# Kernel optimization log

Hardware: AMD Instinct MI355X
Metric: run time of the kernel (lower is better)

Reference implementation:

```python
import jax, jax.numpy as jnp
import numpy as np

SRC_LEN, TGT_LEN, BATCH = 256, 128, 256
NH, NE, NSYM = 512, 256, 64


def setup_inputs() -> dict:
    key = jax.random.key(0)
    ks = jax.random.split(key, 14)
    w = lambda k, shape: jax.random.normal(k, shape, jnp.float32) * 0.05
    return {
        "src_enc": jax.random.normal(ks[0], (SRC_LEN, BATCH, NH), jnp.float32),
        "tgt": jax.random.randint(ks[1], (TGT_LEN, BATCH, 1), 0, NSYM, jnp.int32),
        "src_lengths": jax.random.randint(ks[2], (BATCH,), 1, SRC_LEN + 1, jnp.int32),
        "emb_table": w(ks[3], (NSYM, NE)),
        "Ws_w": w(ks[4], (NH, NH)), "Ws_b": jnp.zeros((NH,), jnp.float32),
        "Wz_w": w(ks[5], (NH, NE + 2 * NH)), "Wz_b": jnp.zeros((NH,), jnp.float32),
        "Wr_w": w(ks[6], (NH, NE + 2 * NH)), "Wr_b": jnp.zeros((NH,), jnp.float32),
        "Wn_w": w(ks[7], (NH, NE + 2 * NH)), "Wn_b": jnp.zeros((NH,), jnp.float32),
        "Wa_w": w(ks[8], (NH, 2 * NH)), "Wa_b": jnp.zeros((NH,), jnp.float32),
        "va_w": w(ks[9], (1, NH)),
        "Wo_w": w(ks[10], (NH, NE + 2 * NH)), "Wo_b": jnp.zeros((NH,), jnp.float32),
    }


def reference(src_enc, tgt, src_lengths, emb_table,
              Ws_w, Ws_b, Wz_w, Wz_b, Wr_w, Wr_b, Wn_w, Wn_b,
              Wa_w, Wa_b, va_w, Wo_w, Wo_b):
    src_len, batch, nh = src_enc.shape
    # src_mask: [src_len, batch] True where position < length
    mask = jnp.arange(src_len)[:, None] < src_lengths[None, :]
    tgt_embed = emb_table[tgt[..., 0]]                     # [T, B, E]
    s0 = jnp.tanh(src_enc[0] @ Ws_w.T + Ws_b)              # [B, H]
    # Split Wa into the s-part and src_enc-part; encoder projection is
    # loop-invariant, compute it once (same math as cat+Linear).
    Wa_s, Wa_e = Wa_w[:, :nh], Wa_w[:, nh:]
    enc_proj = jnp.einsum('sbh,gh->sbg', src_enc, Wa_e) + Wa_b  # [S, B, H]
    va = va_w[0]                                           # [H]
    neg_inf = jnp.float32(-jnp.inf)

    def step(s, emb_i):
        h = jnp.tanh(enc_proj + s @ Wa_s.T)                # [S, B, H]
        ei = jnp.einsum('sbh,h->sb', h, va)                # [S, B]
        ei = jnp.where(mask, ei, neg_inf)
        ai = jax.nn.softmax(ei, axis=0)                    # [S, B]
        ci = jnp.einsum('sb,sbh->bh', ai, src_enc)         # [B, H]
        x = jnp.concatenate([emb_i, s, ci], axis=-1)       # [B, E+2H]
        ti = x @ Wo_w.T + Wo_b
        zi = jax.nn.sigmoid(x @ Wz_w.T + Wz_b)
        ri = jax.nn.sigmoid(x @ Wr_w.T + Wr_b)
        xn = jnp.concatenate([emb_i, ri * s, ci], axis=-1)
        ni = jnp.tanh(xn @ Wn_w.T + Wn_b)
        s_new = (1.0 - zi) * s + zi * ni
        return s_new, (ti, s, ai.T)

    _, (dec_outputs, dec_states, dec_attns) = jax.lax.scan(step, s0, tgt_embed[:-1])
    # dec_outputs/dec_states: [T-1, B, H]; dec_attns: [T-1, B, S]
    return dec_outputs, dec_states, dec_attns
```

## Files before the change

### kernel.cpp

```cpp
#include <hip/hip_runtime.h>
#include <hip/hip_bf16.h>
#include <cstdint>
#include <cstddef>

namespace {

constexpr int S_LEN  = 256;
constexpr int BATCH  = 256;
constexpr int NH     = 512;
constexpr int NE     = 256;
constexpr int NSTEPS = 127;
constexpr int N1     = 2048;
constexpr size_t SB        = (size_t)S_LEN * BATCH;
constexpr size_t SRC_ELEMS = SB * NH;

typedef __attribute__((ext_vector_type(8))) short  short8v;
typedef __attribute__((ext_vector_type(4))) float  float4v;
typedef unsigned short us;

constexpr int EPI_EPROJ = 1, EPI_S0 = 4;

__device__ __forceinline__ float bf2f(us u) {
  union { unsigned int i; float f; } c; c.i = ((unsigned int)u) << 16; return c.f;
}
__device__ __forceinline__ us f2bf(float f) {
  union { float f; unsigned int i; } c; c.f = f;
  unsigned int x = c.i;
  return (us)((x + 0x7FFFu + ((x >> 16) & 1u)) >> 16);
}
__device__ __forceinline__ float tanh2(float x) {
  return 1.f - 2.f * __builtin_amdgcn_rcpf(__expf(2.f * x) + 1.f);
}
__device__ __forceinline__ float sigm(float x) {
  return __builtin_amdgcn_rcpf(1.f + __expf(-x));
}
__device__ __forceinline__ void gload16(const us* g, us* l) {
  __builtin_amdgcn_global_load_lds(
      (const __attribute__((address_space(1))) unsigned int*)g,
      (__attribute__((address_space(3))) unsigned int*)l, 16, 0, 0);
}


__global__ void k_conv_src(const float* __restrict__ src, us* __restrict__ dst) {
  const int total = S_LEN * BATCH * 64;
  int i = blockIdx.x * blockDim.x + threadIdx.x;
  int stride = gridDim.x * blockDim.x;
  for (; i < total; i += stride) {
    int c = i & 63, s = (i >> 6) & 255, b = i >> 14;
    const float* p = src + ((size_t)s * BATCH + b) * NH + c * 8;
    float4 v0 = *(const float4*)p;
    float4 v1 = *(const float4*)(p + 4);
    us o[8] = { f2bf(v0.x), f2bf(v0.y), f2bf(v0.z), f2bf(v0.w),
                f2bf(v1.x), f2bf(v1.y), f2bf(v1.z), f2bf(v1.w) };
    *(short8v*)(dst + (size_t)i * 8) = *(const short8v*)o;
  }
}

__global__ void k_conv_w(const float* __restrict__ Wo, const float* __restrict__ Wz,
                         const float* __restrict__ Wr, const float* __restrict__ Wn,
                         const float* __restrict__ Wa, const float* __restrict__ Ws,
                         const float* __restrict__ Wob, const float* __restrict__ Wzb,
                         const float* __restrict__ Wrb, const float* __restrict__ Wnb,
                         us* __restrict__ W1cat, us* __restrict__ Wns,
                         us* __restrict__ Was, us* __restrict__ Wae,
                         us* __restrict__ Wsbf, float* __restrict__ bcat) {
  const int T1 = 2048 * 1280;
  const int T2 = 512 * 512;
  const int total = T1 + 4 * T2 + 2048;
  int i = blockIdx.x * blockDim.x + threadIdx.x;
  int stride = gridDim.x * blockDim.x;
  for (; i < total; i += stride) {
    int idx = i;
    if (idx < T1) {
      int row = idx / 1280, col = idx - row * 1280;
      float v;
      if      (row < 512)  v = Wo[row * 1280 + col];
      else if (row < 1024) v = Wz[(row - 512) * 1280 + col];
      else if (row < 1536) v = Wr[(row - 1024) * 1280 + col];
      else {
        int g = row - 1536;
        v = (col >= 256 && col < 768) ? 0.f : Wn[g * 1280 + col];
      }
      W1cat[idx] = f2bf(v);
    } else if ((idx -= T1) < T2) {
      int g = idx >> 9, j = idx & 511;
      Wns[idx] = f2bf(Wn[g * 1280 + 256 + j]);
    } else if ((idx -= T2) < T2) {
      int g = idx >> 9, h = idx & 511;
      Was[idx] = f2bf(Wa[g * 1024 + h]);
    } else if ((idx -= T2) < T2) {
      int g = idx >> 9, h = idx & 511;
      Wae[idx] = f2bf(Wa[g * 1024 + 512 + h]);
    } else if ((idx -= T2) < T2) {
      Wsbf[idx] = f2bf(Ws[idx]);
    } else {
      idx -= T2;
      bcat[idx] = (idx < 512) ? Wob[idx]
                : (idx < 1024) ? Wzb[idx - 512]
                : (idx < 1536) ? Wrb[idx - 1024]
                               : Wnb[idx - 1536];
    }
  }
}

__global__ void k_emb(const int* __restrict__ tgt, const float* __restrict__ table,
                      us* __restrict__ emb) {
  const int total = NSTEPS * BATCH * NE;
  int i = blockIdx.x * blockDim.x + threadIdx.x;
  int stride = gridDim.x * blockDim.x;
  for (; i < total; i += stride) {
    int e  = i & (NE - 1);
    int tb = i >> 8;
    int sym = tgt[tb];
    emb[i] = f2bf(table[sym * NE + e]);
  }
}

template<int EPI>
__global__ __launch_bounds__(512, 2) void k_gemm(
    const us* __restrict__ A0, int lda, const us* __restrict__ Bw, int ldb, int K,
    const float* __restrict__ bias, float* __restrict__ f0, us* __restrict__ g0) {
  __shared__ alignas(16) char smem[49152];
  char* As0 = smem;
  char* Bs0 = smem + 16384;
  const int tid = threadIdx.x;
  const int m0 = blockIdx.x * 64, n0 = blockIdx.y * 128;
  const int arow = tid >> 3, ac = (tid & 7) * 8;
  const int brow = tid >> 2, bc = (tid & 3) * 16;
  short8v ar, br0, br1;

  auto loadT = [&](int k0) {
    ar = *(const short8v*)(A0 + (size_t)(m0 + arow) * lda + (k0 + ac));
    const us* q = Bw + (size_t)(n0 + brow) * ldb + (k0 + bc);
    br0 = *(const short8v*)q;
    br1 = *(const short8v*)(q + 8);
  };
  auto stage = [&](int buf) {
    *(short8v*)(As0 + buf * 8192 + arow * 128 + ((ac * 2) ^ ((arow & 7) << 4))) = ar;
    char* bb = Bs0 + buf * 16384 + brow * 128;
    const int sw = (brow & 7) << 4;
    *(short8v*)(bb + ((bc * 2) ^ sw)) = br0;
    *(short8v*)(bb + ((bc * 2 + 16) ^ sw)) = br1;
  };

  const int lane = tid & 63, wave = tid >> 6;
  const int wm = (wave >> 2) * 32, wn = (wave & 3) * 32;
  const int fr = lane & 15, kq = lane >> 4;
  const int ra0 = wm + fr, ra1 = ra0 + 16;
  const int rb0 = wn + fr, rb1 = rb0 + 16;
  float4v acc00 = {0,0,0,0}, acc01 = {0,0,0,0}, acc10 = {0,0,0,0}, acc11 = {0,0,0,0};

  loadT(0);
  stage(0);
  const int nit = K >> 6;
  for (int it = 0; it < nit; ++it) {
    __syncthreads();
    if (it + 1 < nit) loadT((it + 1) << 6);
    const char* ab = As0 + (it & 1) * 8192;
    const char* bb = Bs0 + (it & 1) * 16384;
    #pragma unroll
    for (int ks = 0; ks < 2; ++ks) {
      const int cb = ks * 64 + kq * 16;
      short8v a0 = *(const short8v*)(ab + ra0 * 128 + (cb ^ ((ra0 & 7) << 4)));
      short8v a1 = *(const short8v*)(ab + ra1 * 128 + (cb ^ ((ra1 & 7) << 4)));
      short8v b0 = *(const short8v*)(bb + rb0 * 128 + (cb ^ ((rb0 & 7) << 4)));
      short8v b1 = *(const short8v*)(bb + rb1 * 128 + (cb ^ ((rb1 & 7) << 4)));
      acc00 = __builtin_amdgcn_mfma_f32_16x16x32_bf16(a0, b0, acc00, 0, 0, 0);
      acc01 = __builtin_amdgcn_mfma_f32_16x16x32_bf16(a0, b1, acc01, 0, 0, 0);
      acc10 = __builtin_amdgcn_mfma_f32_16x16x32_bf16(a1, b0, acc10, 0, 0, 0);
      acc11 = __builtin_amdgcn_mfma_f32_16x16x32_bf16(a1, b1, acc11, 0, 0, 0);
    }
    if (it + 1 < nit) stage((it + 1) & 1);
  }

  #pragma unroll
  for (int am = 0; am < 2; ++am) {
    #pragma unroll
    for (int bn = 0; bn < 2; ++bn) {
      float4v a = am ? (bn ? acc11 : acc10) : (bn ? acc01 : acc00);
      #pragma unroll
      for (int r = 0; r < 4; ++r) {
        const int rowO = m0 + wm + am * 16 + kq * 4 + r;
        const int colO = n0 + wn + bn * 16 + fr;
        float v = a[r];
        if (EPI == EPI_S0) {
          float tv = tanh2(v + bias[colO]);
          f0[(size_t)rowO * 512 + colO] = tv;
          g0[(size_t)rowO * 512 + colO] = f2bf(tv);
        } else {
          g0[(size_t)rowO * 512 + colO] = f2bf(v + bias[colO]);
        }
      }
    }
  }
}

__global__ __launch_bounds__(512, 1) void k_fused(
    const us* __restrict__ ep,
    const us* __restrict__ src,
    const us* __restrict__ Wns, const us* __restrict__ Was,
    const float* __restrict__ vaw, const int* __restrict__ slen,
    const float* __restrict__ zi, const float* __restrict__ npart,
    const us* __restrict__ xn,
    float* __restrict__ s_f32, us* __restrict__ s_bf, us* __restrict__ ci_bf,
    float* __restrict__ dec_st_t, float* __restrict__ dec_at_t, int has_gru) {
  __shared__ alignas(16) us stg[3][32][512];
  __shared__ float sfl[512];
  __shared__ float q2l[512];
  __shared__ float pl[256];
  __shared__ float lred[8];
  __shared__ float wpart[8][512];
  const int b = blockIdx.x, tid = threadIdx.x;
  const int lane = tid & 63, wv = tid >> 6;
  const int g0l = lane * 8;
  const int len = slen[b];
  const us* epb  = ep  + (size_t)b * S_LEN * NH;
  const us* srcb = src + (size_t)b * S_LEN * NH;

  float vv2[8]; float sumv = 0.f;
  {
    const float* vp = vaw + g0l;
    #pragma unroll
    for (int j = 0; j < 8; j++) { vv2[j] = 2.f * vp[j]; sumv += vp[j]; }
    #pragma unroll
    for (int off = 32; off > 0; off >>= 1) sumv += __shfl_xor(sumv, off, 64);
  }

  auto issue3 = [&](const us* base) {
    #pragma unroll
    for (int c = 0; c < 3; ++c)
      #pragma unroll
      for (int i = 0; i < 4; ++i) {
        int r = wv * 4 + i;
        gload16(base + (size_t)(c * 32 + r) * NH + g0l, &stg[c][r][0]);
      }
  };

  float s_new;
  if (has_gru) {
    float* xnf = &wpart[0][0];
    xnf[tid] = bf2f(xn[b * 512 + tid]);
    __syncthreads();
    issue3(epb);
    const us* wr = Wns + (size_t)tid * 512;
    float acc = 0.f;
    #pragma unroll 8
    for (int k = 0; k < 64; ++k) {
      short8v w8 = ((const short8v*)wr)[k];
      #pragma unroll
      for (int j = 0; j < 8; j++)
        acc = __builtin_fmaf(bf2f((us)w8[j]), xnf[k * 8 + j], acc);
    }
    float z  = zi[b * 512 + tid];
    float so = s_f32[b * 512 + tid];
    float nv = tanh2(npart[b * 512 + tid] + acc);
    s_new = (1.f - z) * so + z * nv;
    s_f32[b * 512 + tid] = s_new;
    s_bf[b * 512 + tid]  = f2bf(s_new);
  } else {
    issue3(epb);
    s_new = s_f32[b * 512 + tid];
  }
  sfl[tid] = s_new;
  __builtin_nontemporal_store(s_new, &dec_st_t[b * 512 + tid]);
  __syncthreads();

  {
    const us* wr = Was + (size_t)tid * 512;
    float acc = 0.f;
    #pragma unroll 8
    for (int k = 0; k < 64; ++k) {
      short8v w8 = ((const short8v*)wr)[k];
      #pragma unroll
      for (int j = 0; j < 8; j++)
        acc = __builtin_fmaf(bf2f((us)w8[j]), sfl[k * 8 + j], acc);
    }
    q2l[tid] = 2.f * acc;
  }
  __syncthreads();

  float q2[8];
  #pragma unroll
  for (int j = 0; j < 8; j++) q2[j] = q2l[g0l + j];
  float lsum = 0.f;
  #pragma unroll
  for (int c = 0; c < 8; ++c) {
    if (c < 6)      asm volatile("s_waitcnt vmcnt(8)" ::: "memory");
    else if (c == 6) asm volatile("s_waitcnt vmcnt(4)" ::: "memory");
    else             asm volatile("s_waitcnt vmcnt(0)" ::: "memory");
    #pragma unroll
    for (int i = 0; i < 4; ++i) {
      const int r = wv * 4 + i;
      const int s = c * 32 + r;
      short8v v = *(const short8v*)&stg[c % 3][r][g0l];
      float acc = 0.f;
      #pragma unroll
      for (int j = 0; j < 8; j++) {
        float arg = __builtin_fmaf(bf2f((us)v[j]), 2.f, q2[j]);
        acc = __builtin_fmaf(vv2[j], __builtin_amdgcn_rcpf(__expf(arg) + 1.f), acc);
      }
      #pragma unroll
      for (int off = 32; off > 0; off >>= 1) acc += __shfl_xor(acc, off, 64);
      float p = (s < len) ? __expf(sumv - acc) : 0.f;
      if (lane == 0) pl[s] = p;
      lsum += p;
    }
    asm volatile("s_waitcnt lgkmcnt(0)" ::: "memory");
    __builtin_amdgcn_sched_barrier(0);
    if (c + 3 < 8) {
      #pragma unroll
      for (int i = 0; i < 4; ++i) {
        const int r = wv * 4 + i;
        gload16(epb + (size_t)((c + 3) * 32 + r) * NH + g0l, &stg[(c + 3) % 3][r][0]);
      }
    }
  }
  if (lane == 0) lred[wv] = lsum;
  __syncthreads();
  float l = 0.f;
  #pragma unroll
  for (int w = 0; w < 8; w++) l += lred[w];
  const float inv = __builtin_amdgcn_rcpf(l);

  if (tid < 256)
    __builtin_nontemporal_store(pl[tid] * inv, &dec_at_t[b * 256 + tid]);
  issue3(srcb);

  float a8[8] = {0,0,0,0,0,0,0,0};
  #pragma unroll
  for (int c = 0; c < 8; ++c) {
    if (c < 6)      asm volatile("s_waitcnt vmcnt(8)" ::: "memory");
    else if (c == 6) asm volatile("s_waitcnt vmcnt(4)" ::: "memory");
    else             asm volatile("s_waitcnt vmcnt(0)" ::: "memory");
    #pragma unroll
    for (int i = 0; i < 4; ++i) {
      const int r = wv * 4 + i;
      const int s = c * 32 + r;
      short8v v = *(const short8v*)&stg[c % 3][r][g0l];
      float pv = pl[s];
      #pragma unroll
      for (int j = 0; j < 8; j++)
        a8[j] = __builtin_fmaf(pv, bf2f((us)v[j]), a8[j]);
    }
    asm volatile("s_waitcnt lgkmcnt(0)" ::: "memory");
    __builtin_amdgcn_sched_barrier(0);
    if (c + 3 < 8) {
      #pragma unroll
      for (int i = 0; i < 4; ++i) {
        const int r = wv * 4 + i;
        gload16(srcb + (size_t)((c + 3) * 32 + r) * NH + g0l, &stg[(c + 3) % 3][r][0]);
      }
    }
  }
  #pragma unroll
  for (int j = 0; j < 8; j++) wpart[wv][g0l + j] = a8[j];
  __syncthreads();
  float cv = 0.f;
  #pragma unroll
  for (int w = 0; w < 8; w++) cv += wpart[w][tid];
  ci_bf[b * 512 + tid] = f2bf(cv * inv);
}

__global__ __launch_bounds__(256, 4) void k_step1(
    const us* __restrict__ emb_t, const us* __restrict__ sbf,
    const us* __restrict__ cibf, const us* __restrict__ W1cat,
    const float* __restrict__ bcat, const float* __restrict__ s_f32,
    float* __restrict__ dec_out_t, float* __restrict__ zi,
    float* __restrict__ npart, us* __restrict__ xn) {
  __shared__ alignas(16) char smem[24576];
  const int bid = blockIdx.x, tid = threadIdx.x;
  const int lane = tid & 63, wv = tid >> 6;
  char* As = smem;
  char* Bs = smem + 8192;
  const int m0 = (bid >> 4) * 64, n0 = (bid & 15) * 128;
  const int fr = lane & 15, kq = lane >> 4;
  const int wm = (wv & 1) * 32, wn0 = (wv >> 1) * 32;
  const int ra0 = wm + fr, ra1 = ra0 + 16;
  float4v acc[2][2][2];
  #pragma unroll
  for (int x = 0; x < 2; x++)
    #pragma unroll
    for (int y = 0; y < 2; y++)
      #pragma unroll
      for (int z = 0; z < 2; z++) acc[x][y][z] = (float4v){0,0,0,0};

  for (int kt = 0; kt < 20; ++kt) {
    __syncthreads();
    #pragma unroll
    for (int j = 0; j < 2; j++) {
      int cid = tid + 256 * j;
      int arow = cid >> 3, ac8 = (cid & 7) * 8;
      int cc = kt * 64 + ac8, rowg = m0 + arow;
      const us* p = (cc < 256) ? emb_t + (size_t)rowg * 256 + cc
                  : (cc < 768) ? sbf + (size_t)rowg * 512 + (cc - 256)
                               : cibf + (size_t)rowg * 512 + (cc - 768);
      *(short8v*)(As + arow * 128 + ((ac8 * 2) ^ ((arow & 7) << 4))) =
          *(const short8v*)p;
    }
    #pragma unroll
    for (int j = 0; j < 4; j++) {
      int cid = tid + 256 * j;
      int brow = cid >> 3, bc8 = (cid & 7) * 8;
      *(short8v*)(Bs + brow * 128 + ((bc8 * 2) ^ ((brow & 7) << 4))) =
          *(const short8v*)(W1cat + (size_t)(n0 + brow) * 1280 + kt * 64 + bc8);
    }
    __syncthreads();
    #pragma unroll
    for (int ks = 0; ks < 2; ++ks) {
      const int cb = ks * 64 + kq * 16;
      short8v a0 = *(const short8v*)(As + ra0 * 128 + (cb ^ ((ra0 & 7) << 4)));
      short8v a1 = *(const short8v*)(As + ra1 * 128 + (cb ^ ((ra1 & 7) << 4)));
      #pragma unroll
      for (int nh = 0; nh < 2; ++nh) {
        const int rb0 = wn0 + nh * 64 + fr, rb1 = rb0 + 16;
        short8v b0 = *(const short8v*)(Bs + rb0 * 128 + (cb ^ ((rb0 & 7) << 4)));
        short8v b1 = *(const short8v*)(Bs + rb1 * 128 + (cb ^ ((rb1 & 7) << 4)));
        acc[nh][0][0] = __builtin_amdgcn_mfma_f32_16x16x32_bf16(a0, b0, acc[nh][0][0], 0, 0, 0);
        acc[nh][0][1] = __builtin_amdgcn_mfma_f32_16x16x32_bf16(a0, b1, acc[nh][0][1], 0, 0, 0);
        acc[nh][1][0] = __builtin_amdgcn_mfma_f32_16x16x32_bf16(a1, b0, acc[nh][1][0], 0, 0, 0);
        acc[nh][1][1] = __builtin_amdgcn_mfma_f32_16x16x32_bf16(a1, b1, acc[nh][1][1], 0, 0, 0);
      }
    }
  }

  #pragma unroll
  for (int nh = 0; nh < 2; ++nh) {
    #pragma unroll
    for (int am = 0; am < 2; ++am) {
      #pragma unroll
      for (int bn = 0; bn < 2; ++bn) {
        #pragma unroll
        for (int r = 0; r < 4; ++r) {
          const int rowO = m0 + wm + am * 16 + kq * 4 + r;
          const int colO = n0 + wn0 + nh * 64 + bn * 16 + fr;
          float v = acc[nh][am][bn][r] + bcat[colO];
          const int qd = colO >> 9, j = colO & 511;
          const size_t idx = (size_t)rowO * 512 + j;
          if      (qd == 0) __builtin_nontemporal_store(v, &dec_out_t[idx]);
          else if (qd == 1) zi[idx] = sigm(v);
          else if (qd == 2) xn[idx] = f2bf(sigm(v) * s_f32[idx]);
          else              npart[idx] = v;
        }
      }
    }
  }
}

}

extern "C" void kernel_launch(void* const* d_in, const int* in_sizes, int n_in,
                              void* d_out, int out_size, void* d_ws, size_t ws_size,
                              hipStream_t stream) {
  const float* src_enc  = (const float*)d_in[0];
  const int*   tgt      = (const int*)d_in[1];
  const int*   slen     = (const int*)d_in[2];
  const float* emb_tab  = (const float*)d_in[3];
  const float* Wsw      = (const float*)d_in[4];
  const float* Wsb      = (const float*)d_in[5];
  const float* Wzw      = (const float*)d_in[6];
  const float* Wzb      = (const float*)d_in[7];
  const float* Wrw      = (const float*)d_in[8];
  const float* Wrb      = (const float*)d_in[9];
  const float* Wnw      = (const float*)d_in[10];
  const float* Wnb      = (const float*)d_in[11];
  const float* Waw      = (const float*)d_in[12];
  const float* Wab      = (const float*)d_in[13];
  const float* vaw      = (const float*)d_in[14];
  const float* Wow      = (const float*)d_in[15];
  const float* Wob      = (const float*)d_in[16];

  char* ws = (char*)d_ws;
  size_t off = 0;
  auto alloc = [&](size_t bytes) -> void* {
    void* p = ws + off;
    off = (off + bytes + 255) & ~(size_t)255;
    return p;
  };
  us*    src_t  = (us*)alloc(SRC_ELEMS * 2);
  us*    ep_t   = (us*)alloc(SRC_ELEMS * 2);
  us*    emb_bf = (us*)alloc((size_t)NSTEPS * BATCH * NE * 2);
  us*    W1cat  = (us*)alloc((size_t)N1 * 1280 * 2);
  us*    Wns    = (us*)alloc((size_t)512 * 512 * 2);
  us*    Was    = (us*)alloc((size_t)512 * 512 * 2);
  us*    Wae    = (us*)alloc((size_t)512 * 512 * 2);
  us*    Wsbf   = (us*)alloc((size_t)512 * 512 * 2);
  float* bcat   = (float*)alloc((size_t)N1 * 4);
  float* s_f32  = (float*)alloc((size_t)BATCH * NH * 4);
  us*    s_bf   = (us*)alloc((size_t)BATCH * NH * 2);
  float* zi     = (float*)alloc((size_t)BATCH * NH * 4);
  float* npart  = (float*)alloc((size_t)BATCH * NH * 4);
  us*    xn_bf  = (us*)alloc((size_t)BATCH * NH * 2);
  us*    ci_bf  = (us*)alloc((size_t)BATCH * NH * 2);

  float* out         = (float*)d_out;
  float* dec_outputs = out;
  float* dec_states  = out + (size_t)NSTEPS * BATCH * NH;
  float* dec_attns   = dec_states + (size_t)NSTEPS * BATCH * NH;

  k_conv_src<<<4096, 256, 0, stream>>>(src_enc, src_t);
  k_conv_w<<<2048, 256, 0, stream>>>(Wow, Wzw, Wrw, Wnw, Waw, Wsw,
                                     Wob, Wzb, Wrb, Wnb,
                                     W1cat, Wns, Was, Wae, Wsbf, bcat);
  k_emb<<<2048, 256, 0, stream>>>(tgt, emb_tab, emb_bf);
  k_gemm<EPI_S0><<<dim3(4, 4), 512, 0, stream>>>(
      src_t, S_LEN * NH, Wsbf, 512, 512, Wsb, s_f32, s_bf);
  k_gemm<EPI_EPROJ><<<dim3(1024, 4), 512, 0, stream>>>(
      src_t, 512, Wae, 512, 512, Wab, nullptr, ep_t);

  for (int t = 0; t < NSTEPS; t++) {
    k_fused<<<BATCH, 512, 0, stream>>>(
        ep_t, src_t, Wns, Was, vaw, slen, zi, npart, xn_bf,
        s_f32, s_bf, ci_bf,
        dec_states + (size_t)t * BATCH * NH,
        dec_attns + (size_t)t * BATCH * S_LEN, t > 0 ? 1 : 0);
    k_step1<<<64, 256, 0, stream>>>(
        emb_bf + (size_t)t * BATCH * NE, s_bf, ci_bf, W1cat, bcat, s_f32,
        dec_outputs + (size_t)t * BATCH * NH, zi, npart, xn_bf);
  }
}
```

Measured before the change: 11.15 ms.

## Interleave encoder projection and source rows; fuse score and context passes

Stores the bf16 encoder projection and the bf16 source encoding side by side in one row of 1024 elements per (batch, position). The attention kernel then reads both in a single pass over positions, computing unnormalised softmax weights and accumulating the context at once, instead of making two passes through LDS-staged async loads. It drops the LDS staging buffers and raises the occupancy hint so more blocks can hide latency with plain register loads. The context is now accumulated with unnormalised exp weights and scaled by the inverse sum afterwards, which is mathematically the same. The cost is losing the explicit async-copy prefetch pipeline.

```diff
diff --git a/kernel.cpp b/kernel.cpp
--- a/kernel.cpp
+++ b/kernel.cpp
@@ -13,6 +13,7 @@
 constexpr int N1     = 2048;
 constexpr size_t SB        = (size_t)S_LEN * BATCH;
 constexpr size_t SRC_ELEMS = SB * NH;
+constexpr int RW = 1024;
 
 typedef __attribute__((ext_vector_type(8))) short  short8v;
 typedef __attribute__((ext_vector_type(4))) float  float4v;
@@ -34,14 +35,9 @@
 __device__ __forceinline__ float sigm(float x) {
   return __builtin_amdgcn_rcpf(1.f + __expf(-x));
 }
-__device__ __forceinline__ void gload16(const us* g, us* l) {
-  __builtin_amdgcn_global_load_lds(
-      (const __attribute__((address_space(1))) unsigned int*)g,
-      (__attribute__((address_space(3))) unsigned int*)l, 16, 0, 0);
-}
-
-
-__global__ void k_conv_src(const float* __restrict__ src, us* __restrict__ dst) {
+
+
+__global__ void k_conv_src(const float* __restrict__ src, us* __restrict__ cat) {
   const int total = S_LEN * BATCH * 64;
   int i = blockIdx.x * blockDim.x + threadIdx.x;
   int stride = gridDim.x * blockDim.x;
@@ -52,7 +48,8 @@
     float4 v1 = *(const float4*)(p + 4);
     us o[8] = { f2bf(v0.x), f2bf(v0.y), f2bf(v0.z), f2bf(v0.w),
                 f2bf(v1.x), f2bf(v1.y), f2bf(v1.z), f2bf(v1.w) };
-    *(short8v*)(dst + (size_t)i * 8) = *(const short8v*)o;
+    *(short8v*)(cat + ((size_t)b * S_LEN + s) * RW + 512 + c * 8) =
+        *(const short8v*)o;
   }
 }
 
@@ -119,7 +116,8 @@
 template<int EPI>
 __global__ __launch_bounds__(512, 2) void k_gemm(
     const us* __restrict__ A0, int lda, const us* __restrict__ Bw, int ldb, int K,
-    const float* __restrict__ bias, float* __restrict__ f0, us* __restrict__ g0) {
+    const float* __restrict__ bias, float* __restrict__ f0, us* __restrict__ g0,
+    int ldc) {
   __shared__ alignas(16) char smem[49152];
   char* As0 = smem;
   char* Bs0 = smem + 16384;
@@ -186,25 +184,23 @@
         if (EPI == EPI_S0) {
           float tv = tanh2(v + bias[colO]);
           f0[(size_t)rowO * 512 + colO] = tv;
-          g0[(size_t)rowO * 512 + colO] = f2bf(tv);
+          g0[(size_t)rowO * ldc + colO] = f2bf(tv);
         } else {
-          g0[(size_t)rowO * 512 + colO] = f2bf(v + bias[colO]);
+          g0[(size_t)rowO * ldc + colO] = f2bf(v + bias[colO]);
         }
       }
     }
   }
 }
 
-__global__ __launch_bounds__(512, 1) void k_fused(
-    const us* __restrict__ ep,
-    const us* __restrict__ src,
+__global__ __launch_bounds__(512, 4) void k_stepA(
+    const us* __restrict__ cat,
     const us* __restrict__ Wns, const us* __restrict__ Was,
     const float* __restrict__ vaw, const int* __restrict__ slen,
     const float* __restrict__ zi, const float* __restrict__ npart,
     const us* __restrict__ xn,
     float* __restrict__ s_f32, us* __restrict__ s_bf, us* __restrict__ ci_bf,
     float* __restrict__ dec_st_t, float* __restrict__ dec_at_t, int has_gru) {
-  __shared__ alignas(16) us stg[3][32][512];
   __shared__ float sfl[512];
   __shared__ float q2l[512];
   __shared__ float pl[256];
@@ -214,8 +210,6 @@
   const int lane = tid & 63, wv = tid >> 6;
   const int g0l = lane * 8;
   const int len = slen[b];
-  const us* epb  = ep  + (size_t)b * S_LEN * NH;
-  const us* srcb = src + (size_t)b * S_LEN * NH;
 
   float vv2[8]; float sumv = 0.f;
   {
@@ -225,23 +219,12 @@
     #pragma unroll
     for (int off = 32; off > 0; off >>= 1) sumv += __shfl_xor(sumv, off, 64);
   }
-
-  auto issue3 = [&](const us* base) {
-    #pragma unroll
-    for (int c = 0; c < 3; ++c)
-      #pragma unroll
-      for (int i = 0; i < 4; ++i) {
-        int r = wv * 4 + i;
-        gload16(base + (size_t)(c * 32 + r) * NH + g0l, &stg[c][r][0]);
-      }
-  };
 
   float s_new;
   if (has_gru) {
     float* xnf = &wpart[0][0];
     xnf[tid] = bf2f(xn[b * 512 + tid]);
     __syncthreads();
-    issue3(epb);
     const us* wr = Wns + (size_t)tid * 512;
     float acc = 0.f;
     #pragma unroll 8
@@ -257,8 +240,8 @@
     s_new = (1.f - z) * so + z * nv;
     s_f32[b * 512 + tid] = s_new;
     s_bf[b * 512 + tid]  = f2bf(s_new);
+    __syncthreads();
   } else {
-    issue3(epb);
     s_new = s_f32[b * 512 + tid];
   }
   sfl[tid] = s_new;
@@ -282,40 +265,55 @@
   float q2[8];
   #pragma unroll
   for (int j = 0; j < 8; j++) q2[j] = q2l[g0l + j];
+
+  const us* cb = cat + (size_t)b * S_LEN * RW + g0l;
   float lsum = 0.f;
-  #pragma unroll
-  for (int c = 0; c < 8; ++c) {
-    if (c < 6)      asm volatile("s_waitcnt vmcnt(8)" ::: "memory");
-    else if (c == 6) asm volatile("s_waitcnt vmcnt(4)" ::: "memory");
-    else             asm volatile("s_waitcnt vmcnt(0)" ::: "memory");
-    #pragma unroll
-    for (int i = 0; i < 4; ++i) {
-      const int r = wv * 4 + i;
-      const int s = c * 32 + r;
-      short8v v = *(const short8v*)&stg[c % 3][r][g0l];
-      float acc = 0.f;
-      #pragma unroll
-      for (int j = 0; j < 8; j++) {
-        float arg = __builtin_fmaf(bf2f((us)v[j]), 2.f, q2[j]);
-        acc = __builtin_fmaf(vv2[j], __builtin_amdgcn_rcpf(__expf(arg) + 1.f), acc);
-      }
-      #pragma unroll
-      for (int off = 32; off > 0; off >>= 1) acc += __shfl_xor(acc, off, 64);
-      float p = (s < len) ? __expf(sumv - acc) : 0.f;
-      if (lane == 0) pl[s] = p;
-      lsum += p;
-    }
-    asm volatile("s_waitcnt lgkmcnt(0)" ::: "memory");
-    __builtin_amdgcn_sched_barrier(0);
-    if (c + 3 < 8) {
-      #pragma unroll
-      for (int i = 0; i < 4; ++i) {
-        const int r = wv * 4 + i;
-        gload16(epb + (size_t)((c + 3) * 32 + r) * NH + g0l, &stg[(c + 3) % 3][r][0]);
-      }
-    }
-  }
+  float c8a = 0.f, c8b = 0.f, c8c = 0.f, c8d = 0.f,
+        c8e = 0.f, c8f = 0.f, c8g = 0.f, c8h = 0.f;
+
+  short8v e0, f0, e1, f1, e2, f2, e3, f3;
+  auto LDR = [&](int i, short8v& ev, short8v& fv) {
+    const us* p = cb + (size_t)(wv + 8 * i) * RW;
+    ev = *(const short8v*)p;
+    fv = *(const short8v*)(p + 512);
+  };
+  auto PROC = [&](int i, short8v& ev, short8v& fv) {
+    const int s = wv + 8 * i;
+    float acc = 0.f;
+    #pragma unroll
+    for (int j = 0; j < 8; j++) {
+      float arg = __builtin_fmaf(bf2f((us)ev[j]), 2.f, q2[j]);
+      acc = __builtin_fmaf(vv2[j], __builtin_amdgcn_rcpf(__expf(arg) + 1.f), acc);
+    }
+    #pragma unroll
+    for (int off = 32; off > 0; off >>= 1) acc += __shfl_xor(acc, off, 64);
+    float p = (s < len) ? __expf(sumv - acc) : 0.f;
+    if (lane == 0) pl[s] = p;
+    lsum += p;
+    c8a = __builtin_fmaf(p, bf2f((us)fv[0]), c8a);
+    c8b = __builtin_fmaf(p, bf2f((us)fv[1]), c8b);
+    c8c = __builtin_fmaf(p, bf2f((us)fv[2]), c8c);
+    c8d = __builtin_fmaf(p, bf2f((us)fv[3]), c8d);
+    c8e = __builtin_fmaf(p, bf2f((us)fv[4]), c8e);
+    c8f = __builtin_fmaf(p, bf2f((us)fv[5]), c8f);
+    c8g = __builtin_fmaf(p, bf2f((us)fv[6]), c8g);
+    c8h = __builtin_fmaf(p, bf2f((us)fv[7]), c8h);
+  };
+
+  LDR(0, e0, f0); LDR(1, e1, f1); LDR(2, e2, f2); LDR(3, e3, f3);
+  for (int i = 0; i < 32; i += 4) {
+    PROC(i + 0, e0, f0); if (i + 4 < 32) LDR(i + 4, e0, f0);
+    PROC(i + 1, e1, f1); if (i + 5 < 32) LDR(i + 5, e1, f1);
+    PROC(i + 2, e2, f2); if (i + 6 < 32) LDR(i + 6, e2, f2);
+    PROC(i + 3, e3, f3); if (i + 7 < 32) LDR(i + 7, e3, f3);
+  }
+
   if (lane == 0) lred[wv] = lsum;
+  {
+    float w0_[8] = { c8a, c8b, c8c, c8d, c8e, c8f, c8g, c8h };
+    #pragma unroll
+    for (int j = 0; j < 8; j++) wpart[wv][g0l + j] = w0_[j];
+  }
   __syncthreads();
   float l = 0.f;
   #pragma unroll
@@ -324,44 +322,14 @@
 
   if (tid < 256)
     __builtin_nontemporal_store(pl[tid] * inv, &dec_at_t[b * 256 + tid]);
-  issue3(srcb);
-
-  float a8[8] = {0,0,0,0,0,0,0,0};
-  #pragma unroll
-  for (int c = 0; c < 8; ++c) {
-    if (c < 6)      asm volatile("s_waitcnt vmcnt(8)" ::: "memory");
-    else if (c == 6) asm volatile("s_waitcnt vmcnt(4)" ::: "memory");
-    else             asm volatile("s_waitcnt vmcnt(0)" ::: "memory");
-    #pragma unroll
-    for (int i = 0; i < 4; ++i) {
-      const int r = wv * 4 + i;
-      const int s = c * 32 + r;
-      short8v v = *(const short8v*)&stg[c % 3][r][g0l];
-      float pv = pl[s];
-      #pragma unroll
-      for (int j = 0; j < 8; j++)
-        a8[j] = __builtin_fmaf(pv, bf2f((us)v[j]), a8[j]);
-    }
-    asm volatile("s_waitcnt lgkmcnt(0)" ::: "memory");
-    __builtin_amdgcn_sched_barrier(0);
-    if (c + 3 < 8) {
-      #pragma unroll
-      for (int i = 0; i < 4; ++i) {
-        const int r = wv * 4 + i;
-        gload16(srcb + (size_t)((c + 3) * 32 + r) * NH + g0l, &stg[(c + 3) % 3][r][0]);
-      }
-    }
-  }
-  #pragma unroll
-  for (int j = 0; j < 8; j++) wpart[wv][g0l + j] = a8[j];
-  __syncthreads();
+
   float cv = 0.f;
   #pragma unroll
   for (int w = 0; w < 8; w++) cv += wpart[w][tid];
   ci_bf[b * 512 + tid] = f2bf(cv * inv);
 }
 
-__global__ __launch_bounds__(256, 4) void k_step1(
+__global__ __launch_bounds__(256, 4) void k_stepB(
     const us* __restrict__ emb_t, const us* __restrict__ sbf,
     const us* __restrict__ cibf, const us* __restrict__ W1cat,
     const float* __restrict__ bcat, const float* __restrict__ s_f32,
@@ -476,8 +444,7 @@
     off = (off + bytes + 255) & ~(size_t)255;
     return p;
   };
-  us*    src_t  = (us*)alloc(SRC_ELEMS * 2);
-  us*    ep_t   = (us*)alloc(SRC_ELEMS * 2);
+  us*    cat    = (us*)alloc(SB * RW * 2);
   us*    emb_bf = (us*)alloc((size_t)NSTEPS * BATCH * NE * 2);
   us*    W1cat  = (us*)alloc((size_t)N1 * 1280 * 2);
   us*    Wns    = (us*)alloc((size_t)512 * 512 * 2);
@@ -497,23 +464,23 @@
   float* dec_states  = out + (size_t)NSTEPS * BATCH * NH;
   float* dec_attns   = dec_states + (size_t)NSTEPS * BATCH * NH;
 
-  k_conv_src<<<4096, 256, 0, stream>>>(src_enc, src_t);
+  k_conv_src<<<4096, 256, 0, stream>>>(src_enc, cat);
   k_conv_w<<<2048, 256, 0, stream>>>(Wow, Wzw, Wrw, Wnw, Waw, Wsw,
                                      Wob, Wzb, Wrb, Wnb,
                                      W1cat, Wns, Was, Wae, Wsbf, bcat);
   k_emb<<<2048, 256, 0, stream>>>(tgt, emb_tab, emb_bf);
   k_gemm<EPI_S0><<<dim3(4, 4), 512, 0, stream>>>(
-      src_t, S_LEN * NH, Wsbf, 512, 512, Wsb, s_f32, s_bf);
+      cat + 512, S_LEN * RW, Wsbf, 512, 512, Wsb, s_f32, s_bf, 512);
   k_gemm<EPI_EPROJ><<<dim3(1024, 4), 512, 0, stream>>>(
-      src_t, 512, Wae, 512, 512, Wab, nullptr, ep_t);
+      cat + 512, RW, Wae, 512, 512, Wab, nullptr, cat, RW);
 
   for (int t = 0; t < NSTEPS; t++) {
-    k_fused<<<BATCH, 512, 0, stream>>>(
-        ep_t, src_t, Wns, Was, vaw, slen, zi, npart, xn_bf,
+    k_stepA<<<BATCH, 512, 0, stream>>>(
+        cat, Wns, Was, vaw, slen, zi, npart, xn_bf,
         s_f32, s_bf, ci_bf,
         dec_states + (size_t)t * BATCH * NH,
         dec_attns + (size_t)t * BATCH * S_LEN, t > 0 ? 1 : 0);
-    k_step1<<<64, 256, 0, stream>>>(
+    k_stepB<<<64, 256, 0, stream>>>(
         emb_bf + (size_t)t * BATCH * NE, s_bf, ci_bf, W1cat, bcat, s_f32,
         dec_outputs + (size_t)t * BATCH * NH, zi, npart, xn_bf);
   }
```

Result: faster. 10.67 ms (-4.3%).
